# Optimization experiments

Hardware: AMD Instinct MI355X
Metric: run time of the kernel (lower is better)

The kernel has to match this reference:

```python
import jax, jax.numpy as jnp
import numpy as np

N_TARGET = 1_000_000
GRID = 220
C_IN, C_OUT = 32, 64
BN_EPS = 1e-5


def _build_topology():
    # Real sparse-voxel topology: random occupied cells in a GRID^3 volume.
    rng = np.random.default_rng(0)
    raw = rng.integers(0, GRID, size=(1_400_000, 3), dtype=np.int64)
    keys = np.unique((raw[:, 0] * GRID + raw[:, 1]) * GRID + raw[:, 2])[:N_TARGET]
    N = keys.shape[0]
    coords = np.stack([keys // (GRID * GRID), (keys // GRID) % GRID, keys % GRID], axis=1)
    # Rulebook: for each of the 27 kernel offsets, index of the neighbor voxel (N = missing -> zero pad row).
    nbr = np.full((N, 27), N, dtype=np.int32)
    k = 0
    for dx in (-1, 0, 1):
        for dy in (-1, 0, 1):
            for dz in (-1, 0, 1):
                nc = coords + np.array([dx, dy, dz])
                valid = np.all((nc >= 0) & (nc < GRID), axis=1)
                nk = (nc[:, 0] * GRID + nc[:, 1]) * GRID + nc[:, 2]
                pos = np.clip(np.searchsorted(keys, nk), 0, N - 1)
                found = valid & (keys[pos] == nk)
                nbr[found, k] = pos[found].astype(np.int32)
                k += 1
    # MaxPool(2,2): voxels sharing coords//2 pool together.
    PG = GRID // 2 + 1
    pkeys = ((coords[:, 0] // 2) * PG + coords[:, 1] // 2) * PG + coords[:, 2] // 2
    uniq, pool_ids = np.unique(pkeys, return_inverse=True)
    return N, nbr, pool_ids.astype(np.int32), int(uniq.shape[0])


def setup_inputs() -> dict:
    N, nbr, pool_ids, num_pooled = _build_topology()
    key = jax.random.key(0)
    k1, k2, k3 = jax.random.split(key, 3)
    return {
        "feats": jax.random.normal(k1, (N, C_IN), dtype=jnp.float32),
        "W1": jax.random.normal(k2, (27, C_IN, C_OUT), dtype=jnp.float32) * 0.1,
        "gamma1": jnp.ones((C_OUT,), jnp.float32),
        "beta1": jnp.zeros((C_OUT,), jnp.float32),
        "W2": jax.random.normal(k3, (27, C_OUT, C_OUT), dtype=jnp.float32) * 0.1,
        "gamma2": jnp.ones((C_OUT,), jnp.float32),
        "beta2": jnp.zeros((C_OUT,), jnp.float32),
        "nbr_idx": jnp.asarray(nbr),
        "pool_ids": jnp.asarray(pool_ids),
        "num_pooled": num_pooled,
    }


def _sparse_conv3(f, W, nbr_idx):
    # f: [N, Cin], W: [27, Cin, Cout], nbr_idx: [N, 27] with pad index N.
    N = f.shape[0]
    fp = jnp.concatenate([f, jnp.zeros((1, f.shape[1]), f.dtype)], axis=0)  # zero pad row
    out = jnp.zeros((N, W.shape[2]), f.dtype)
    for k in range(27):  # fixed kernel offsets: gather -> GEMM -> accumulate
        out = out + fp[nbr_idx[:, k]] @ W[k]
    return out


def _batch_norm(f, gamma, beta):
    # Training-mode BN over the voxel dim (biased variance), as torch BatchNorm.
    m = f.mean(axis=0)
    v = f.var(axis=0)
    return (f - m) * jax.lax.rsqrt(v + BN_EPS) * gamma + beta


def reference(feats, W1, gamma1, beta1, W2, gamma2, beta2, nbr_idx, pool_ids, num_pooled):
    x = jax.nn.relu(_batch_norm(_sparse_conv3(feats, W1, nbr_idx), gamma1, beta1))
    x = _batch_norm(_sparse_conv3(x, W2, nbr_idx), gamma2, beta2)
    pooled = jax.ops.segment_max(x, pool_ids, num_segments=num_pooled)
    return x, pooled
```

## Files before the change

kernel.cpp:

```cpp
#include <hip/hip_runtime.h>
#include <hip/hip_bf16.h>
#include <stdint.h>

#define TPB 256

typedef __bf16 bf16x8 __attribute__((ext_vector_type(8)));
typedef float f32x4 __attribute__((ext_vector_type(4)));
union U16x8 { uint4 u; bf16x8 b; };

typedef const uint32_t __attribute__((address_space(1))) glb_u32;
typedef uint32_t __attribute__((address_space(3))) lds_u32;

__device__ __forceinline__ float bfbits2f(uint32_t lo16) {
  union { uint32_t u; float f; } c; c.u = lo16 << 16; return c.f;
}
__device__ __forceinline__ uint16_t f2bf_rne(float f) {
  union { float f; uint32_t u; } c; c.f = f;
  uint32_t r = 0x7FFFu + ((c.u >> 16) & 1u);
  return (uint16_t)((c.u + r) >> 16);
}

__global__ __launch_bounds__(TPB) void prep_w_kernel(
    const float* __restrict__ W1, const float* __restrict__ W2,
    uint16_t* __restrict__ w1t, uint16_t* __restrict__ w2t)
{
  int i = blockIdx.x * TPB + threadIdx.x;
  if (i < 27 * 2048) {
    int k = i >> 11, cin = (i >> 6) & 31, cout = i & 63;
    int cin2 = (((cin >> 3) ^ (cout & 3)) << 3) | (cin & 7);
    w1t[(k << 11) + (cout << 5) + cin2] = f2bf_rne(W1[i]);
  } else {
    int j = i - 27 * 2048;
    if (j < 27 * 4096) {
      int k = j >> 12, cin = (j >> 6) & 63, cout = j & 63;
      int cin2 = (((cin >> 3) ^ (cout & 7)) << 3) | (cin & 7);
      w2t[(k << 12) + (cout << 6) + cin2] = f2bf_rne(W2[j]);
    }
  }
}

__global__ __launch_bounds__(TPB) void prep_x0_kernel(
    const float* __restrict__ feats, uint16_t* __restrict__ x0, long long N)
{
  long long t = (long long)blockIdx.x * TPB + threadIdx.x;
  if (t >= (N + 1) * 4) return;
  long long e = t * 8;
  uint4 o;
  if (e < N * 32) {
    float4 a = *(const float4*)(feats + e);
    float4 b = *(const float4*)(feats + e + 4);
    o.x = (uint32_t)f2bf_rne(a.x) | ((uint32_t)f2bf_rne(a.y) << 16);
    o.y = (uint32_t)f2bf_rne(a.z) | ((uint32_t)f2bf_rne(a.w) << 16);
    o.z = (uint32_t)f2bf_rne(b.x) | ((uint32_t)f2bf_rne(b.y) << 16);
    o.w = (uint32_t)f2bf_rne(b.z) | ((uint32_t)f2bf_rne(b.w) << 16);
  } else {
    o.x = o.y = o.z = o.w = 0;
  }
  *(uint4*)(x0 + e) = o;
}

__global__ __launch_bounds__(TPB) void bucket_build_kernel(
    const int* __restrict__ pool_ids, int* __restrict__ count,
    int* __restrict__ members, long long N)
{
  long long i = (long long)blockIdx.x * TPB + threadIdx.x;
  if (i < N) {
    int pid = pool_ids[i];
    int slot = atomicAdd(&count[pid], 1);
    members[(long long)pid * 8 + slot] = (int)i;
  }
}

template <int CIN, int R, int OCC>
__global__ __launch_bounds__(TPB, OCC) void conv_mfma_kernel(
    const uint16_t* __restrict__ x, const uint16_t* __restrict__ wt,
    const int* __restrict__ nbr, uint16_t* __restrict__ yb,
    float* __restrict__ statsrep, int N)
{
  constexpr int CHUNKS = CIN / 32;
  constexpr int LOGROWB = (CIN == 32) ? 6 : 7;
  constexpr int SWZ = (CIN == 32) ? 3 : 7;
  constexpr int WKB = 64 * CIN * 2;
  constexpr int NW = WKB / (TPB * 16);
  constexpr int ROWS = 4 * R * 16;
  constexpr int NINTS = ROWS * 27;
  constexpr int NCH16 = NINTS / 4;

  __shared__ __align__(16) char Wlds[4][WKB];
  __shared__ __align__(16) int nbrLds[NINTS];
  __shared__ float sred[4][128];

  const int tid = threadIdx.x;
  const int lane = tid & 63;
  const int wave = tid >> 6;
  const int l15 = lane & 15;
  const int l4 = lane >> 4;

  int bid;
  {
    int nwg = gridDim.x, q = nwg >> 3, r = nwg & 7;
    int xcd = blockIdx.x & 7, pos = blockIdx.x >> 3;
    bid = (xcd < r ? xcd * (q + 1) : r * (q + 1) + (xcd - r) * q) + pos;
  }
  const long long row0 = (long long)bid * ROWS;

  f32x4 acc[R][4];
#pragma unroll
  for (int r = 0; r < R; ++r)
#pragma unroll
    for (int t = 0; t < 4; ++t)
      acc[r][t] = (f32x4){0.f, 0.f, 0.f, 0.f};

  {
    const char* nsrc = (const char*)nbr + row0 * 108;
    long long blkB = (long long)N * 108 - row0 * 108;
    int fullChunks = (int)(blkB >> 4);
    if (fullChunks > NCH16) fullChunks = NCH16;
#pragma unroll
    for (int u = 0; u < (NCH16 + TPB - 1) / TPB; ++u) {
      int idx = u * TPB + tid;
      if (idx < fullChunks)
        __builtin_amdgcn_global_load_lds((glb_u32*)(nsrc + idx * 16),
                                         (lds_u32*)((char*)nbrLds + idx * 16), 16, 0, 0);
    }
    for (int ii = fullChunks * 4 + tid; ii < NINTS; ii += TPB) {
      long long gi = row0 * 27 + ii;
      nbrLds[ii] = (gi < (long long)N * 27) ? nbr[gi] : N;
    }
  }

  auto stageW = [&](int k, int slot) {
    const char* src = (const char*)(wt + (size_t)k * 64 * CIN);
#pragma unroll
    for (int u = 0; u < NW; ++u) {
      int off = (tid + u * TPB) * 16;
      __builtin_amdgcn_global_load_lds((glb_u32*)(src + off),
                                       (lds_u32*)(&Wlds[slot][off]), 16, 0, 0);
    }
  };
  auto gather = [&](int k, U16x8 (&dst)[R][CHUNKS]) {
#pragma unroll
    for (int r = 0; r < R; ++r) {
      int lrow = (wave * R + r) * 16 + l15;
      int g = nbrLds[lrow * 27 + k];
      const uint16_t* xr = x + (size_t)g * CIN + (l4 << 3);
#pragma unroll
      for (int c = 0; c < CHUNKS; ++c)
        dst[r][c].u = *(const uint4*)(xr + c * 32);
    }
  };
  auto compute = [&](int slot, U16x8 (&xs)[R][CHUNKS]) {
    bf16x8 bfrag[4][CHUNKS];
#pragma unroll
    for (int t = 0; t < 4; ++t) {
      int n = t * 16 + l15;
#pragma unroll
      for (int c = 0; c < CHUNKS; ++c) {
        int colb = (l4 << 4) + (c << 6);
        int d = (n << LOGROWB) | (colb ^ ((n & SWZ) << 4));
        U16x8 tmp; tmp.u = *(const uint4*)(&Wlds[slot][d]);
        bfrag[t][c] = tmp.b;
      }
    }
#pragma unroll
    for (int r = 0; r < R; ++r)
#pragma unroll
      for (int c = 0; c < CHUNKS; ++c)
#pragma unroll
        for (int t = 0; t < 4; ++t)
          acc[r][t] = __builtin_amdgcn_mfma_f32_16x16x32_bf16(
              xs[r][c].b, bfrag[t][c], acc[r][t], 0, 0, 0);
  };

  U16x8 xPe[R][CHUNKS], xPo[R][CHUNKS], xQe[R][CHUNKS], xQo[R][CHUNKS];

  stageW(0, 0); stageW(1, 1);
  __syncthreads();
  gather(0, xPe); gather(1, xPo);

#pragma unroll 1
  for (int t = 0; t < 6; ++t) {
    const int k4 = 4 * t;
    __syncthreads();
    stageW(k4 + 2, 2); stageW(k4 + 3, 3);
    gather(k4 + 2, xQe); gather(k4 + 3, xQo);
    compute(0, xPe);
    compute(1, xPo);
    __syncthreads();
    stageW(k4 + 4, 0); stageW(k4 + 5, 1);
    gather(k4 + 4, xPe); gather(k4 + 5, xPo);
    compute(2, xQe);
    compute(3, xQo);
  }
  __syncthreads();
  stageW(26, 2);
  gather(26, xQe);
  compute(0, xPe);
  compute(1, xPo);
  __syncthreads();
  compute(2, xQe);

#pragma unroll
  for (int r = 0; r < R; ++r) {
    long long vr0 = row0 + (wave * R + r) * 16 + (l4 << 2);
#pragma unroll
    for (int reg = 0; reg < 4; ++reg) {
      long long vr = vr0 + reg;
      if (vr < N) {
        uint16_t* yr = yb + vr * 64 + l15;
#pragma unroll
        for (int t = 0; t < 4; ++t) yr[t * 16] = f2bf_rne(acc[r][t][reg]);
      }
    }
  }

  float s[4], s2[4];
#pragma unroll
  for (int t = 0; t < 4; ++t) { s[t] = 0.f; s2[t] = 0.f; }
#pragma unroll
  for (int r = 0; r < R; ++r) {
    long long vr0 = row0 + (wave * R + r) * 16 + (l4 << 2);
#pragma unroll
    for (int reg = 0; reg < 4; ++reg) {
      if (vr0 + reg < N) {
#pragma unroll
        for (int t = 0; t < 4; ++t) {
          float v = acc[r][t][reg];
          s[t] += v;
          s2[t] = fmaf(v, v, s2[t]);
        }
      }
    }
  }
#pragma unroll
  for (int t = 0; t < 4; ++t) {
    s[t] += __shfl_xor(s[t], 16);
    s[t] += __shfl_xor(s[t], 32);
    s2[t] += __shfl_xor(s2[t], 16);
    s2[t] += __shfl_xor(s2[t], 32);
  }
  __syncthreads();
  if (l4 == 0) {
#pragma unroll
    for (int t = 0; t < 4; ++t) {
      sred[wave][t * 16 + l15] = s[t];
      sred[wave][64 + t * 16 + l15] = s2[t];
    }
  }
  __syncthreads();
  if (tid < 128) {
    float tot = sred[0][tid] + sred[1][tid] + sred[2][tid] + sred[3][tid];
    atomicAdd(&statsrep[(bid & 15) * 128 + tid], tot);
  }
}

__global__ void bn_finalize_kernel(const float* __restrict__ reps,
                                   float* __restrict__ fin, float n)
{
  int c = threadIdx.x;
  float s = 0.f, s2 = 0.f;
  for (int r = 0; r < 16; ++r) { s += reps[r * 128 + c]; s2 += reps[r * 128 + 64 + c]; }
  float mean = s / n;
  float var = s2 / n - mean * mean;
  fin[c] = mean;
  fin[64 + c] = rsqrtf(var + 1e-5f);
}

__global__ __launch_bounds__(TPB) void bn_relu_bf16_kernel(
    const uint16_t* __restrict__ yb, const float* __restrict__ fin,
    const float* __restrict__ gamma, const float* __restrict__ beta,
    uint16_t* __restrict__ x1, long long N)
{
  long long e = ((long long)blockIdx.x * TPB + threadIdx.x) * 8;
  if (e >= (N + 1) * 64) return;
  long long row = e >> 6;
  int c = (int)(e & 63);
  uint4 out;
  if (row < N) {
    uint4 v = *(const uint4*)(yb + e);
    const uint32_t vv[4] = {v.x, v.y, v.z, v.w};
    uint32_t res[4];
#pragma unroll
    for (int q = 0; q < 4; ++q) {
      int cc = c + q * 2;
      float a0 = bfbits2f(vv[q] & 0xFFFFu);
      float a1 = bfbits2f(vv[q] >> 16);
      float o0 = fmaf((a0 - fin[cc]) * fin[64 + cc], gamma[cc], beta[cc]);
      float o1 = fmaf((a1 - fin[cc + 1]) * fin[64 + cc + 1], gamma[cc + 1], beta[cc + 1]);
      o0 = o0 > 0.f ? o0 : 0.f;
      o1 = o1 > 0.f ? o1 : 0.f;
      res[q] = (uint32_t)f2bf_rne(o0) | ((uint32_t)f2bf_rne(o1) << 16);
    }
    out.x = res[0]; out.y = res[1]; out.z = res[2]; out.w = res[3];
  } else {
    out.x = out.y = out.z = out.w = 0;
  }
  *(uint4*)(x1 + e) = out;
}

__global__ __launch_bounds__(TPB) void pool_max_write_kernel(
    const uint16_t* __restrict__ yb, const float* __restrict__ fin,
    const float* __restrict__ gamma, const float* __restrict__ beta,
    const int* __restrict__ count, const int* __restrict__ members,
    float* __restrict__ xout, float* __restrict__ pooled, long long P)
{
  long long pid = (long long)blockIdx.x * 16 + (threadIdx.x >> 4);
  if (pid >= P) return;
  int c0 = (threadIdx.x & 15) * 4;
  float4 m = *(const float4*)(fin + c0);
  float4 r = *(const float4*)(fin + 64 + c0);
  float4 g = *(const float4*)(gamma + c0);
  float4 b = *(const float4*)(beta + c0);
  int cnt = count[pid];
  float4 acc = {-3.4e38f, -3.4e38f, -3.4e38f, -3.4e38f};
  const int* mem = members + pid * 8;
  for (int t = 0; t < cnt; ++t) {
    long long row = mem[t];
    ushort4 v = *(const ushort4*)(yb + row * 64 + c0);
    float4 o;
    o.x = fmaf((bfbits2f(v.x) - m.x) * r.x, g.x, b.x);
    o.y = fmaf((bfbits2f(v.y) - m.y) * r.y, g.y, b.y);
    o.z = fmaf((bfbits2f(v.z) - m.z) * r.z, g.z, b.z);
    o.w = fmaf((bfbits2f(v.w) - m.w) * r.w, g.w, b.w);
    *(float4*)(xout + row * 64 + c0) = o;
    acc.x = fmaxf(acc.x, o.x);
    acc.y = fmaxf(acc.y, o.y);
    acc.z = fmaxf(acc.z, o.z);
    acc.w = fmaxf(acc.w, o.w);
  }
  *(float4*)(pooled + pid * 64 + c0) = acc;
}

extern "C" void kernel_launch(void* const* d_in, const int* in_sizes, int n_in,
                              void* d_out, int out_size, void* d_ws, size_t ws_size,
                              hipStream_t stream)
{
  const float* feats  = (const float*)d_in[0];
  const float* W1     = (const float*)d_in[1];
  const float* gamma1 = (const float*)d_in[2];
  const float* beta1  = (const float*)d_in[3];
  const float* W2     = (const float*)d_in[4];
  const float* gamma2 = (const float*)d_in[5];
  const float* beta2  = (const float*)d_in[6];
  const int* nbr      = (const int*)d_in[7];
  const int* pool_ids = (const int*)d_in[8];

  const long long N = (long long)in_sizes[0] / 32;
  const long long P = (long long)out_size / 64 - N;

  char* ws = (char*)d_ws;
  uint16_t* yb = (uint16_t*)ws;
  size_t y_bytes = ((size_t)N * 64 * 2 + 255) & ~(size_t)255;
  char* regB = ws + y_bytes;
  size_t regB_bytes = ((size_t)(N + 1) * 64 * 2 + 255) & ~(size_t)255;
  uint16_t* x0 = (uint16_t*)regB;
  uint16_t* x1 = (uint16_t*)regB;
  float* reps1 = (float*)(regB + regB_bytes);
  float* reps2 = reps1 + 16 * 128;
  float* fin1 = reps2 + 16 * 128;
  float* fin2 = fin1 + 128;
  int* count   = (int*)(fin2 + 128);
  int* members = count + P;

  float* xout = (float*)d_out;
  float* pooled = xout + (size_t)N * 64;
  uint16_t* w1t = (uint16_t*)pooled;
  uint16_t* w2t = w1t + 27 * 2048;

  hipMemsetAsync(reps1, 0, 2 * 16 * 128 * sizeof(float), stream);
  hipMemsetAsync(count, 0, (size_t)P * 4, stream);

  prep_w_kernel<<<(27 * 2048 + 27 * 4096 + TPB - 1) / TPB, TPB, 0, stream>>>(W1, W2, w1t, w2t);
  prep_x0_kernel<<<(int)(((N + 1) * 4 + TPB - 1) / TPB), TPB, 0, stream>>>(feats, x0, N);
  bucket_build_kernel<<<(int)((N + TPB - 1) / TPB), TPB, 0, stream>>>(pool_ids, count, members, N);

  const int convBlocks = (int)((N + 127) / 128);
  conv_mfma_kernel<32, 2, 4><<<convBlocks, TPB, 0, stream>>>(x0, w1t, nbr, yb, reps1, (int)N);
  bn_finalize_kernel<<<1, 64, 0, stream>>>(reps1, fin1, (float)N);

  long long t1 = ((N + 1) * 64) / 8;
  bn_relu_bf16_kernel<<<(int)((t1 + TPB - 1) / TPB), TPB, 0, stream>>>(
      yb, fin1, gamma1, beta1, x1, N);

  conv_mfma_kernel<64, 2, 3><<<convBlocks, TPB, 0, stream>>>(x1, w2t, nbr, yb, reps2, (int)N);
  bn_finalize_kernel<<<1, 64, 0, stream>>>(reps2, fin2, (float)N);

  pool_max_write_kernel<<<(int)((P + 15) / 16), TPB, 0, stream>>>(
      yb, fin2, gamma2, beta2, count, members, xout, pooled, P);
}
```

Before: 706.2 us.

## Stage contiguous neighbor-row windows in LDS instead of per-lane global gathers

The convolution now computes, for each group of three kernel offsets (the same dx,dy), the minimum neighbor index across the block and stages a contiguous window of 176 feature rows into LDS. The MFMA operand is read from that window, with a fallback to a direct global load for neighbors outside it. The feature buffers are written with an XOR swizzle so these LDS reads avoid bank conflicts. This replaces scattered global gathers with bulk async loads, but costs more LDS (occupancy hints drop), uses a single-stage weight double buffer, and can add divergent fallback loads.

Measured after the change: 860.0 us. 21.8% more time.

```diff
diff --git a/kernel.cpp b/kernel.cpp
--- a/kernel.cpp
+++ b/kernel.cpp
@@ -45,6 +45,8 @@
   long long t = (long long)blockIdx.x * TPB + threadIdx.x;
   if (t >= (N + 1) * 4) return;
   long long e = t * 8;
+  long long row = e >> 5;
+  int slot = (int)(e >> 3) & 3;
   uint4 o;
   if (e < N * 32) {
     float4 a = *(const float4*)(feats + e);
@@ -56,7 +58,8 @@
   } else {
     o.x = o.y = o.z = o.w = 0;
   }
-  *(uint4*)(x0 + e) = o;
+  long long dst = row * 32 + ((slot ^ ((int)row & 3)) << 3);
+  *(uint4*)(x0 + dst) = o;
 }
 
 __global__ __launch_bounds__(TPB) void bucket_build_kernel(
@@ -78,17 +81,23 @@
     float* __restrict__ statsrep, int N)
 {
   constexpr int CHUNKS = CIN / 32;
-  constexpr int LOGROWB = (CIN == 32) ? 6 : 7;
+  constexpr int ROWB = CIN * 2;
   constexpr int SWZ = (CIN == 32) ? 3 : 7;
   constexpr int WKB = 64 * CIN * 2;
   constexpr int NW = WKB / (TPB * 16);
   constexpr int ROWS = 4 * R * 16;
   constexpr int NINTS = ROWS * 27;
   constexpr int NCH16 = NINTS / 4;
-
-  __shared__ __align__(16) char Wlds[4][WKB];
+  constexpr int WCAP = 176;
+  constexpr int PADROW = 176;
+  constexpr int WROWS = 177;
+  constexpr int XNI = (WCAP * ROWB + TPB * 16 - 1) / (TPB * 16);
+
+  __shared__ __align__(16) char Wlds[2][WKB];
+  __shared__ __align__(16) char Xlds[2][WROWS * ROWB];
   __shared__ __align__(16) int nbrLds[NINTS];
   __shared__ float sred[4][128];
+  __shared__ int winloLds[9];
 
   const int tid = threadIdx.x;
   const int lane = tid & 63;
@@ -129,76 +138,101 @@
     }
   }
 
-  auto stageW = [&](int k, int slot) {
+  auto stageW = [&](int k, int b) {
     const char* src = (const char*)(wt + (size_t)k * 64 * CIN);
 #pragma unroll
     for (int u = 0; u < NW; ++u) {
       int off = (tid + u * TPB) * 16;
       __builtin_amdgcn_global_load_lds((glb_u32*)(src + off),
-                                       (lds_u32*)(&Wlds[slot][off]), 16, 0, 0);
+                                       (lds_u32*)(&Wlds[b][off]), 16, 0, 0);
     }
   };
-  auto gather = [&](int k, U16x8 (&dst)[R][CHUNKS]) {
+  auto xstage = [&](int j, int xb) {
+    int wl = winloLds[j];
+    int rows = N + 1 - wl; if (rows > WCAP) rows = WCAP;
+    int bytes = rows * ROWB;
+    const char* src = (const char*)x + (size_t)wl * ROWB;
+#pragma unroll
+    for (int u = 0; u < XNI; ++u) {
+      int idx = (u * TPB + tid) * 16;
+      if (idx < bytes)
+        __builtin_amdgcn_global_load_lds((glb_u32*)(src + idx),
+                                         (lds_u32*)(&Xlds[xb][idx]), 16, 0, 0);
+    }
+  };
+  auto compute = [&](int wsel, int xb, int k) {
+    const int wl = winloLds[k / 3];
+    bf16x8 bfrag[4][CHUNKS];
+#pragma unroll
+    for (int t = 0; t < 4; ++t) {
+      int n = t * 16 + l15;
+#pragma unroll
+      for (int c = 0; c < CHUNKS; ++c) {
+        int colb = (l4 << 4) + (c << 6);
+        int d = n * ROWB + (colb ^ ((n & SWZ) << 4));
+        U16x8 tmp; tmp.u = *(const uint4*)(&Wlds[wsel][d]);
+        bfrag[t][c] = tmp.b;
+      }
+    }
 #pragma unroll
     for (int r = 0; r < R; ++r) {
       int lrow = (wave * R + r) * 16 + l15;
       int g = nbrLds[lrow * 27 + k];
-      const uint16_t* xr = x + (size_t)g * CIN + (l4 << 3);
-#pragma unroll
-      for (int c = 0; c < CHUNKS; ++c)
-        dst[r][c].u = *(const uint4*)(xr + c * 32);
-    }
-  };
-  auto compute = [&](int slot, U16x8 (&xs)[R][CHUNKS]) {
-    bf16x8 bfrag[4][CHUNKS];
-#pragma unroll
-    for (int t = 0; t < 4; ++t) {
-      int n = t * 16 + l15;
+      int d = g - wl;
+      bool pad = (g == N);
+      bool inw = (unsigned)d < (unsigned)WCAP;
+      int sc = (pad || !inw) ? PADROW : d;
+      U16x8 xf[CHUNKS];
 #pragma unroll
       for (int c = 0; c < CHUNKS; ++c) {
-        int colb = (l4 << 4) + (c << 6);
-        int d = (n << LOGROWB) | (colb ^ ((n & SWZ) << 4));
-        U16x8 tmp; tmp.u = *(const uint4*)(&Wlds[slot][d]);
-        bfrag[t][c] = tmp.b;
+        int slot = l4 + 4 * c;
+        int off = sc * ROWB + ((slot ^ (sc & SWZ)) << 4);
+        xf[c].u = *(const uint4*)(&Xlds[xb][off]);
       }
-    }
-#pragma unroll
-    for (int r = 0; r < R; ++r)
+      if (!pad && !inw) {
+#pragma unroll
+        for (int c = 0; c < CHUNKS; ++c) {
+          int slot = l4 + 4 * c;
+          xf[c].u = *(const uint4*)(x + (size_t)g * CIN + ((slot ^ (g & SWZ)) << 3));
+        }
+      }
 #pragma unroll
       for (int c = 0; c < CHUNKS; ++c)
 #pragma unroll
         for (int t = 0; t < 4; ++t)
           acc[r][t] = __builtin_amdgcn_mfma_f32_16x16x32_bf16(
-              xs[r][c].b, bfrag[t][c], acc[r][t], 0, 0, 0);
+              xf[c].b, bfrag[t][c], acc[r][t], 0, 0, 0);
+    }
   };
 
-  U16x8 xPe[R][CHUNKS], xPo[R][CHUNKS], xQe[R][CHUNKS], xQo[R][CHUNKS];
-
-  stageW(0, 0); stageW(1, 1);
+  stageW(0, 0);
   __syncthreads();
-  gather(0, xPe); gather(1, xPo);
+
+  for (int j = wave; j < 9; j += 4) {
+    int m = N;
+#pragma unroll
+    for (int d = 0; d < 3; ++d) {
+      m = min(m, nbrLds[lane * 27 + 3 * j + d]);
+      m = min(m, nbrLds[(lane + 64) * 27 + 3 * j + d]);
+    }
+#pragma unroll
+    for (int off = 32; off; off >>= 1) m = min(m, __shfl_xor(m, off));
+    if (lane == 0) winloLds[j] = m & ~7;
+  }
+  if (tid < 2 * (ROWB / 16)) {
+    int b = tid / (ROWB / 16), q = tid % (ROWB / 16);
+    *(uint4*)(&Xlds[b][PADROW * ROWB + q * 16]) = (uint4){0, 0, 0, 0};
+  }
+  __syncthreads();
+  xstage(0, 0);
 
 #pragma unroll 1
-  for (int t = 0; t < 6; ++t) {
-    const int k4 = 4 * t;
+  for (int k = 0; k < 27; ++k) {
     __syncthreads();
-    stageW(k4 + 2, 2); stageW(k4 + 3, 3);
-    gather(k4 + 2, xQe); gather(k4 + 3, xQo);
-    compute(0, xPe);
-    compute(1, xPo);
-    __syncthreads();
-    stageW(k4 + 4, 0); stageW(k4 + 5, 1);
-    gather(k4 + 4, xPe); gather(k4 + 5, xPo);
-    compute(2, xQe);
-    compute(3, xQo);
-  }
-  __syncthreads();
-  stageW(26, 2);
-  gather(26, xQe);
-  compute(0, xPe);
-  compute(1, xPo);
-  __syncthreads();
-  compute(2, xQe);
+    if (k + 1 < 27) stageW(k + 1, (k + 1) & 1);
+    if ((k % 3) == 0 && k + 3 < 27) xstage(k / 3 + 1, (k / 3 + 1) & 1);
+    compute(k & 1, (k / 3) & 1, k);
+  }
 
 #pragma unroll
   for (int r = 0; r < R; ++r) {
@@ -271,9 +305,11 @@
     const float* __restrict__ gamma, const float* __restrict__ beta,
     uint16_t* __restrict__ x1, long long N)
 {
-  long long e = ((long long)blockIdx.x * TPB + threadIdx.x) * 8;
-  if (e >= (N + 1) * 64) return;
+  long long t = (long long)blockIdx.x * TPB + threadIdx.x;
+  if (t >= (N + 1) * 8) return;
+  long long e = t * 8;
   long long row = e >> 6;
+  int slot = (int)(e >> 3) & 7;
   int c = (int)(e & 63);
   uint4 out;
   if (row < N) {
@@ -295,7 +331,8 @@
   } else {
     out.x = out.y = out.z = out.w = 0;
   }
-  *(uint4*)(x1 + e) = out;
+  long long dst = row * 64 + ((slot ^ ((int)row & 7)) << 3);
+  *(uint4*)(x1 + dst) = out;
 }
 
 __global__ __launch_bounds__(TPB) void pool_max_write_kernel(
@@ -375,14 +412,14 @@
   bucket_build_kernel<<<(int)((N + TPB - 1) / TPB), TPB, 0, stream>>>(pool_ids, count, members, N);
 
   const int convBlocks = (int)((N + 127) / 128);
-  conv_mfma_kernel<32, 2, 4><<<convBlocks, TPB, 0, stream>>>(x0, w1t, nbr, yb, reps1, (int)N);
+  conv_mfma_kernel<32, 2, 3><<<convBlocks, TPB, 0, stream>>>(x0, w1t, nbr, yb, reps1, (int)N);
   bn_finalize_kernel<<<1, 64, 0, stream>>>(reps1, fin1, (float)N);
 
-  long long t1 = ((N + 1) * 64) / 8;
+  long long t1 = (N + 1) * 8;
   bn_relu_bf16_kernel<<<(int)((t1 + TPB - 1) / TPB), TPB, 0, stream>>>(
       yb, fin1, gamma1, beta1, x1, N);
 
-  conv_mfma_kernel<64, 2, 3><<<convBlocks, TPB, 0, stream>>>(x1, w2t, nbr, yb, reps2, (int)N);
+  conv_mfma_kernel<64, 2, 2><<<convBlocks, TPB, 0, stream>>>(x1, w2t, nbr, yb, reps2, (int)N);
   bn_finalize_kernel<<<1, 64, 0, stream>>>(reps2, fin2, (float)N);
 
   pool_max_write_kernel<<<(int)((P + 15) / 16), TPB, 0, stream>>>(
```

## Switch conv weight staging to two-slot double buffering with explicit vmcnt waits

Applied to the files above, without the earlier changes.

The 27-offset conv main loop moves from four weight LDS slots and four register gather buffers (two offsets per stage) to a two-slot ping-pong. Each stage loads the next offset's weights and gathers while computing the current one, then synchronises with a targeted s_waitcnt vmcnt plus barrier instead of a full __syncthreads. This halves weight LDS usage and gather register buffers, aiming for more occupancy and cheaper synchronisation. The trade-off is a shallower prefetch pipeline, which may expose gather latency.

Result: no change. 693.3 us (-1.8%).

```diff
diff --git a/kernel.cpp b/kernel.cpp
--- a/kernel.cpp
+++ b/kernel.cpp
@@ -10,6 +10,12 @@
 
 typedef const uint32_t __attribute__((address_space(1))) glb_u32;
 typedef uint32_t __attribute__((address_space(3))) lds_u32;
+
+template <int N> __device__ __forceinline__ void stage_wait_barrier() {
+  asm volatile("s_waitcnt vmcnt(%0)" :: "i"(N) : "memory");
+  __builtin_amdgcn_s_barrier();
+  __builtin_amdgcn_sched_barrier(0);
+}
 
 __device__ __forceinline__ float bfbits2f(uint32_t lo16) {
   union { uint32_t u; float f; } c; c.u = lo16 << 16; return c.f;
@@ -82,11 +88,12 @@
   constexpr int SWZ = (CIN == 32) ? 3 : 7;
   constexpr int WKB = 64 * CIN * 2;
   constexpr int NW = WKB / (TPB * 16);
+  constexpr int NG = R * CHUNKS;
   constexpr int ROWS = 4 * R * 16;
   constexpr int NINTS = ROWS * 27;
   constexpr int NCH16 = NINTS / 4;
 
-  __shared__ __align__(16) char Wlds[4][WKB];
+  __shared__ __align__(16) char Wlds[2][WKB];
   __shared__ __align__(16) int nbrLds[NINTS];
   __shared__ float sred[4][128];
 
@@ -129,13 +136,13 @@
     }
   }
 
-  auto stageW = [&](int k, int slot) {
+  auto stageW = [&](int k, int b) {
     const char* src = (const char*)(wt + (size_t)k * 64 * CIN);
 #pragma unroll
     for (int u = 0; u < NW; ++u) {
       int off = (tid + u * TPB) * 16;
       __builtin_amdgcn_global_load_lds((glb_u32*)(src + off),
-                                       (lds_u32*)(&Wlds[slot][off]), 16, 0, 0);
+                                       (lds_u32*)(&Wlds[b][off]), 16, 0, 0);
     }
   };
   auto gather = [&](int k, U16x8 (&dst)[R][CHUNKS]) {
@@ -149,7 +156,7 @@
         dst[r][c].u = *(const uint4*)(xr + c * 32);
     }
   };
-  auto compute = [&](int slot, U16x8 (&xs)[R][CHUNKS]) {
+  auto compute = [&](int wsel, U16x8 (&xs)[R][CHUNKS]) {
     bf16x8 bfrag[4][CHUNKS];
 #pragma unroll
     for (int t = 0; t < 4; ++t) {
@@ -158,7 +165,7 @@
       for (int c = 0; c < CHUNKS; ++c) {
         int colb = (l4 << 4) + (c << 6);
         int d = (n << LOGROWB) | (colb ^ ((n & SWZ) << 4));
-        U16x8 tmp; tmp.u = *(const uint4*)(&Wlds[slot][d]);
+        U16x8 tmp; tmp.u = *(const uint4*)(&Wlds[wsel][d]);
         bfrag[t][c] = tmp.b;
       }
     }
@@ -172,33 +179,26 @@
               xs[r][c].b, bfrag[t][c], acc[r][t], 0, 0, 0);
   };
 
-  U16x8 xPe[R][CHUNKS], xPo[R][CHUNKS], xQe[R][CHUNKS], xQo[R][CHUNKS];
-
-  stageW(0, 0); stageW(1, 1);
+  U16x8 xA[R][CHUNKS], xB[R][CHUNKS];
+
+  stageW(0, 0);
   __syncthreads();
-  gather(0, xPe); gather(1, xPo);
+  gather(0, xA);
 
 #pragma unroll 1
-  for (int t = 0; t < 6; ++t) {
-    const int k4 = 4 * t;
-    __syncthreads();
-    stageW(k4 + 2, 2); stageW(k4 + 3, 3);
-    gather(k4 + 2, xQe); gather(k4 + 3, xQo);
-    compute(0, xPe);
-    compute(1, xPo);
-    __syncthreads();
-    stageW(k4 + 4, 0); stageW(k4 + 5, 1);
-    gather(k4 + 4, xPe); gather(k4 + 5, xPo);
-    compute(2, xQe);
-    compute(3, xQo);
-  }
-  __syncthreads();
-  stageW(26, 2);
-  gather(26, xQe);
-  compute(0, xPe);
-  compute(1, xPo);
-  __syncthreads();
-  compute(2, xQe);
+  for (int kk = 0; kk < 13; ++kk) {
+    stageW(2 * kk + 1, 1);
+    __builtin_amdgcn_sched_barrier(0);
+    gather(2 * kk + 1, xB);
+    compute(0, xA);
+    stage_wait_barrier<NG>();
+    stageW(2 * kk + 2, 0);
+    __builtin_amdgcn_sched_barrier(0);
+    gather(2 * kk + 2, xA);
+    compute(1, xB);
+    stage_wait_barrier<NG>();
+  }
+  compute(0, xA);
 
 #pragma unroll
   for (int r = 0; r < R; ++r) {
```
